# Kernel optimization log

Hardware: AMD Instinct MI355X
Metric: run time of the kernel (lower is better)

## Reference

```python
import jax, jax.numpy as jnp
import numpy as np
from jax import lax

DN = ('NHWC', 'HWIO', 'NHWC')


def conv_same(x, w):
    return lax.conv_general_dilated(x, w, window_strides=(1, 1), padding='SAME',
                                    dimension_numbers=DN)


def dwconv(x, w):
    # w: (kh, kw, F, 1) TF depthwise layout -> HWIO (kh, kw, 1, F), groups=F
    F = w.shape[2]
    return lax.conv_general_dilated(x, jnp.transpose(w, (0, 1, 3, 2)),
                                    window_strides=(1, 1), padding='SAME',
                                    dimension_numbers=DN, feature_group_count=F)


def hard_sigmoid(x):
    return jnp.clip(0.2 * x + 0.5, 0.0, 1.0)


def setup_inputs() -> dict:
    key = jax.random.key(0)
    ks = jax.random.split(key, 10)
    B, H, W, Cin, F = 16, 128, 128, 64, 64
    s = 0.05
    return {
        'inputs': jax.random.normal(ks[0], (B, H, W, Cin), jnp.float32),
        'h0': jax.random.normal(ks[1], (B, H, W, F), jnp.float32),
        'c0': jax.random.normal(ks[2], (B, H, W, F), jnp.float32),
        'm0': jax.random.normal(ks[3], (B, H, W, F), jnp.float32),
        'kernel': jax.random.normal(ks[4], (3, 3, Cin, 4 * F), jnp.float32) * s,
        'recurrent_kernel': jax.random.normal(ks[5], (3, 3, F, 4 * F), jnp.float32) * s,
        'bias': jnp.concatenate([jnp.zeros((F,), jnp.float32),
                                 jnp.ones((F,), jnp.float32),
                                 jnp.zeros((2 * F,), jnp.float32)]),
        'sa_kernel': jax.random.normal(ks[6], (1, 1, F, 5), jnp.float32) * s,
        'kernel_z': jax.random.normal(ks[7], (3, 3, 2, F), jnp.float32) * s,
        'depth_wise_kernel': jax.random.normal(ks[8], (3, 3, F, 6), jnp.float32) * s,
        'sa_bias': jnp.zeros((3 * F,), jnp.float32),
    }


def reference(inputs, h0, c0, m0, kernel, recurrent_kernel, bias, sa_kernel,
              kernel_z, depth_wise_kernel, sa_bias):
    F = h0.shape[-1]
    # --- ConvLSTM gates (no dropout: all four gates share the same input, so
    # a single fused conv over the 4F-channel kernel is the same math) ---
    xz = conv_same(inputs, kernel) + bias  # [B,H,W,4F]
    hz = conv_same(h0, recurrent_kernel)   # [B,H,W,4F]
    z = xz + hz
    zi_, zf_, zc_, zo_ = jnp.split(z, 4, axis=-1)
    i = hard_sigmoid(zi_)
    f = hard_sigmoid(zf_)
    c = f * c0 + i * jnp.tanh(zc_)
    o = hard_sigmoid(zo_)
    h = o * jnp.tanh(c)  # [B,H,W,F]

    # --- Self-attention memory (SAM) module; 1x1 convs -> channel contractions ---
    w = sa_kernel[0, 0]  # [F,5]
    v_h = jnp.einsum('bhwc,c->bhw', h, w[:, 0])
    k_h = jnp.einsum('bhwc,c->bhw', h, w[:, 1])
    q_h = jnp.einsum('bhwc,c->bhw', h, w[:, 2])
    k_m = jnp.einsum('bhwc,c->bhw', m0, w[:, 3])
    v_m = jnp.einsum('bhwc,c->bhw', m0, w[:, 4])

    alpha_m = jax.nn.softmax(jnp.matmul(q_h, k_m), axis=-1)  # [B,H,H] (H==W)
    alpha_h = jax.nn.softmax(jnp.matmul(q_h, k_h), axis=-1)
    z_m = jnp.matmul(alpha_m, v_m)  # [B,H,W]
    z_h = jnp.matmul(alpha_h, v_h)

    zi = conv_same(jnp.stack([z_h, z_m], axis=-1), kernel_z)  # [B,H,W,F]

    dw = depth_wise_kernel  # [3,3,F,6]
    b_i, b_g, b_o = jnp.split(sa_bias, 3)
    i2 = jax.nn.sigmoid(dwconv(zi, dw[..., 0:1]) + dwconv(h, dw[..., 1:2]) + b_i)
    g = jnp.tanh(dwconv(zi, dw[..., 2:3]) + dwconv(h, dw[..., 3:4]) + b_g)
    o2 = jax.nn.sigmoid(dwconv(zi, dw[..., 4:5]) + dwconv(h, dw[..., 5:6]) + b_o)

    m_t = (1.0 - i2) * m0 + i2 * g
    h_hat = m_t * o2
    return h_hat, c, m_t
```

## Files before the change

### kernel.cpp

```cpp
#include <hip/hip_runtime.h>

#define BB 16
#define HH 128
#define WW 128
#define FF 64
#define NPIX (BB*HH*WW)

typedef short bf16x8 __attribute__((ext_vector_type(8)));
typedef float f32x4 __attribute__((ext_vector_type(4)));

__device__ __forceinline__ float bf2f(unsigned int u){ return __uint_as_float(u<<16); }
__device__ __forceinline__ unsigned short f2bf(float f){
  unsigned u = __float_as_uint(f);
  u += 0x7fffu + ((u>>16)&1u);
  return (unsigned short)(u>>16);
}
__device__ __forceinline__ float hsig(float x){ return fminf(fmaxf(fmaf(0.2f,x,0.5f),0.f),1.f); }
__device__ __forceinline__ float tanh_fast(float x){
  float e = __expf(2.f*x);
  return 1.f - 2.f/(e + 1.f);
}
__device__ __forceinline__ void gload_lds16(const void* g, void* l){
  __builtin_amdgcn_global_load_lds(
      (const __attribute__((address_space(1))) unsigned int*)g,
      (__attribute__((address_space(3))) unsigned int*)l, 16, 0, 0);
}

__global__ __launch_bounds__(256) void zero_pads(unsigned short* __restrict__ Xp){
  int i = blockIdx.x*256 + threadIdx.x;
  if (i >= 16*516) return;
  int b = i / 516, r = i % 516;
  int y, x;
  if (r < 130){ y = 0; x = r; }
  else if (r < 260){ y = 129; x = r-130; }
  else if (r < 388){ y = r-260+1; x = 0; }
  else { y = r-388+1; x = 129; }
  unsigned short* p = Xp + (((size_t)(b*130 + y)*130) + x)*128;
  uint4 z = {0u,0u,0u,0u};
  #pragma unroll
  for (int c=0;c<16;++c) ((uint4*)p)[c] = z;
}

__global__ __launch_bounds__(256) void prep_x(const float* __restrict__ in,
                                              const float* __restrict__ h0,
                                              unsigned short* __restrict__ Xp){
  int gi = blockIdx.x*256 + threadIdx.x;
  int pix = gi >> 4;
  int ch8 = (gi & 15) * 8;
  const float* src = (ch8 < 64) ? (in + (size_t)pix*64 + ch8)
                                : (h0 + (size_t)pix*64 + (ch8-64));
  float4 v0 = *(const float4*)src;
  float4 v1 = *(const float4*)(src+4);
  uint4 o;
  o.x = (unsigned)f2bf(v0.x) | ((unsigned)f2bf(v0.y)<<16);
  o.y = (unsigned)f2bf(v0.z) | ((unsigned)f2bf(v0.w)<<16);
  o.z = (unsigned)f2bf(v1.x) | ((unsigned)f2bf(v1.y)<<16);
  o.w = (unsigned)f2bf(v1.z) | ((unsigned)f2bf(v1.w)<<16);
  int b = pix >> 14, y = (pix >> 7) & 127, x = pix & 127;
  *(uint4*)(Xp + (((size_t)(b*130 + y+1)*130) + (x+1))*128 + ch8) = o;
}

__global__ __launch_bounds__(256) void prep_w(const float* __restrict__ kern,
                                              const float* __restrict__ rkern,
                                              unsigned short* __restrict__ Wg){
  int k = blockIdx.x;
  int n = threadIdx.x;
  int tap = k >> 7, c = k & 127;
  float v = (c < 64) ? kern[((size_t)(tap*64 + c))*256 + n]
                     : rkern[((size_t)(tap*64 + (c-64)))*256 + n];
  Wg[(size_t)n*1152 + k] = f2bf(v);
}

__global__ __launch_bounds__(256, 2) void gates_kernel(
    const unsigned short* __restrict__ Xp,
    const unsigned short* __restrict__ Wg,
    const float* __restrict__ bias,
    const float* __restrict__ c0,
    float* __restrict__ c_out,
    unsigned short* __restrict__ h_bf){
  __shared__ unsigned short As[2][130*128];
  const int gid = blockIdx.x;
  const int swz = (gid & 7)*256 + (gid >> 3);
  const int b  = swz >> 7;
  const int y  = swz & 127;
  const int tid = threadIdx.x;
  const int l = tid & 63;
  const int wid = tid >> 6;
  const int l15 = l & 15, l4 = l >> 4;
  const int n0 = wid*16 + l15;

  const unsigned short* brow[4];
  #pragma unroll
  for (int g=0; g<4; ++g) brow[g] = Wg + (size_t)(g*64 + n0)*1152 + l4*8;

  f32x4 acc[8][4];
  #pragma unroll
  for (int mf=0;mf<8;++mf)
    #pragma unroll
    for (int g=0;g<4;++g) acc[mf][g] = (f32x4){0.f,0.f,0.f,0.f};

  auto stage = [&](int buf, int dyi){
    const unsigned short* gbase = Xp + ((size_t)((b*130 + y + dyi)*130))*128;
    unsigned short* lbase = &As[buf][0];
    #pragma unroll
    for (int it=0; it<8; ++it){
      int q = it*256 + tid;
      int px = q >> 4, c = q & 15;
      int cs = c ^ (px & 7);
      gload_lds16(gbase + (size_t)px*128 + cs*8, lbase + (size_t)q*8);
    }
    if (l < 8){
      int q = 2048 + wid*8 + l;
      int px = q >> 4, c = q & 15;
      int cs = c ^ (px & 7);
      gload_lds16(gbase + (size_t)px*128 + cs*8, lbase + (size_t)q*8);
    }
  };

  stage(0, 0);
  for (int dyi = 0; dyi < 3; ++dyi){
    if (dyi < 2){
      stage((dyi+1)&1, dyi+1);
      asm volatile("s_waitcnt vmcnt(9)" ::: "memory");
    } else {
      asm volatile("s_waitcnt vmcnt(0)" ::: "memory");
    }
    __builtin_amdgcn_sched_barrier(0);
    __builtin_amdgcn_s_barrier();
    __builtin_amdgcn_sched_barrier(0);
    const unsigned short* asb = &As[dyi&1][0];
    #pragma unroll
    for (int dxi = 0; dxi < 3; ++dxi){
      const int tap = dyi*3 + dxi;
      #pragma unroll
      for (int ksc = 0; ksc < 2; ++ksc){
        bf16x8 bfr[4][2];
        #pragma unroll
        for (int g=0; g<4; ++g)
          #pragma unroll
          for (int k2=0; k2<2; ++k2)
            bfr[g][k2] = *(const bf16x8*)(brow[g] + tap*128 + (ksc*2+k2)*32);
        #pragma unroll
        for (int k2=0; k2<2; ++k2){
          const int cd = (ksc*2+k2)*4 + l4;
          #pragma unroll
          for (int mf=0; mf<8; ++mf){
            const int px = mf*16 + l15 + dxi;
            bf16x8 a = *(const bf16x8*)(asb + (size_t)px*128 + ((cd ^ (px & 7))*8));
            #pragma unroll
            for (int g=0;g<4;++g)
              acc[mf][g] = __builtin_amdgcn_mfma_f32_16x16x32_bf16(a, bfr[g][k2], acc[mf][g], 0,0,0);
          }
        }
      }
    }
    __builtin_amdgcn_sched_barrier(0);
    __builtin_amdgcn_s_barrier();
    __builtin_amdgcn_sched_barrier(0);
  }
  const float b0 = bias[n0], b1 = bias[64+n0], b2 = bias[128+n0], b3 = bias[192+n0];
  const size_t prow = (size_t)(b*128 + y)*128;
  #pragma unroll
  for (int mf=0;mf<8;++mf){
    #pragma unroll
    for (int r=0;r<4;++r){
      const int x = mf*16 + l4*4 + r;
      const size_t p = prow + x;
      const float zi_ = acc[mf][0][r] + b0;
      const float zf_ = acc[mf][1][r] + b1;
      const float zc_ = acc[mf][2][r] + b2;
      const float zo_ = acc[mf][3][r] + b3;
      const float iv = hsig(zi_), fv = hsig(zf_), ov = hsig(zo_);
      const float cv = fv*c0[p*64 + n0] + iv*tanh_fast(zc_);
      const float hv = ov*tanh_fast(cv);
      c_out[p*64 + n0] = cv;
      h_bf[p*64 + n0] = f2bf(hv);
    }
  }
}

__global__ __launch_bounds__(256) void qkv_kernel(
    const unsigned short* __restrict__ h_bf, const float* __restrict__ m0,
    const float* __restrict__ sak,
    float* __restrict__ q_h, float* __restrict__ k_h, float* __restrict__ v_h,
    float* __restrict__ k_m, float* __restrict__ v_m){
  __shared__ float wS[320];
  for (int i = threadIdx.x; i < 320; i += 256) wS[i] = sak[i];
  __syncthreads();
  const int p = blockIdx.x*256 + threadIdx.x;
  const unsigned short* hp = h_bf + (size_t)p*64;
  const float* mp = m0 + (size_t)p*64;
  float a0=0,a1=0,a2=0,a3=0,a4=0;
  #pragma unroll
  for (int ch = 0; ch < 64; ch += 8){
    uint4 hu = *(const uint4*)(hp + ch);
    float4 ma = *(const float4*)(mp + ch);
    float4 mb = *(const float4*)(mp + ch + 4);
    float hv[8] = { bf2f(hu.x&0xffffu), bf2f(hu.x>>16), bf2f(hu.y&0xffffu), bf2f(hu.y>>16),
                    bf2f(hu.z&0xffffu), bf2f(hu.z>>16), bf2f(hu.w&0xffffu), bf2f(hu.w>>16) };
    float mv[8] = { ma.x,ma.y,ma.z,ma.w, mb.x,mb.y,mb.z,mb.w };
    #pragma unroll
    for (int jj=0;jj<8;++jj){
      const float* w = &wS[(ch+jj)*5];
      a0 = fmaf(hv[jj], w[0], a0);
      a1 = fmaf(hv[jj], w[1], a1);
      a2 = fmaf(hv[jj], w[2], a2);
      a3 = fmaf(mv[jj], w[3], a3);
      a4 = fmaf(mv[jj], w[4], a4);
    }
  }
  v_h[p]=a0; k_h[p]=a1; q_h[p]=a2; k_m[p]=a3; v_m[p]=a4;
}

__global__ __launch_bounds__(256) void attn_kernel(
    const float* __restrict__ q_h, const float* __restrict__ k_h, const float* __restrict__ v_h,
    const float* __restrict__ k_m, const float* __restrict__ v_m,
    float* __restrict__ z_h, float* __restrict__ z_m){
  __shared__ float Kl[128][132];
  __shared__ float Vl[128][132];
  __shared__ float q2[8][132];
  __shared__ float al[8][132];
  const int bid = blockIdx.x;
  const int b = bid >> 4;
  const int type = (bid >> 3) & 1;
  const int rb = bid & 7;
  const float* K = (type ? k_m : k_h) + (size_t)b*16384;
  const float* V = (type ? v_m : v_h) + (size_t)b*16384;
  const float* Q = q_h + (size_t)b*16384;
  float* Z = (type ? z_m : z_h) + (size_t)b*16384;
  const int t = threadIdx.x;
  const int jq = t & 31;
  const int r8 = t >> 5;

  for (int base = 0; base < 16384; base += 1024){
    const int idx = base + t*4;
    const int w = idx >> 7, j = idx & 127;
    const float4 kv = *(const float4*)(K + idx);
    const float4 vv = *(const float4*)(V + idx);
    *(float4*)&Kl[w][j] = kv;
    *(float4*)&Vl[w][j] = vv;
  }

  for (int p = 0; p < 2; ++p){
    __syncthreads();
    for (int idx = t; idx < 1024; idx += 256)
      q2[idx>>7][idx&127] = Q[(rb*16 + p*8 + (idx>>7))*128 + (idx&127)];
    __syncthreads();
    const int i = rb*16 + p*8 + r8;
    float s0=0.f,s1=0.f,s2=0.f,s3=0.f;
    #pragma unroll 8
    for (int w=0; w<128; ++w){
      const float qv = q2[r8][w];
      const float4 kv = *(const float4*)&Kl[w][jq*4];
      s0 = fmaf(qv, kv.x, s0); s1 = fmaf(qv, kv.y, s1);
      s2 = fmaf(qv, kv.z, s2); s3 = fmaf(qv, kv.w, s3);
    }
    float mx = fmaxf(fmaxf(s0,s1), fmaxf(s2,s3));
    #pragma unroll
    for (int o=1;o<32;o<<=1) mx = fmaxf(mx, __shfl_xor(mx, o));
    const float p0 = __expf(s0-mx), p1 = __expf(s1-mx);
    const float p2 = __expf(s2-mx), p3 = __expf(s3-mx);
    float sm = (p0+p1)+(p2+p3);
    #pragma unroll
    for (int o=1;o<32;o<<=1) sm += __shfl_xor(sm, o);
    const float inv = 1.f/sm;
    *(float4*)&al[r8][jq*4] = make_float4(p0*inv, p1*inv, p2*inv, p3*inv);
    __syncthreads();
    float z0=0.f,z1=0.f,z2=0.f,z3=0.f;
    #pragma unroll 8
    for (int w=0; w<128; ++w){
      const float av = al[r8][w];
      const float4 vv = *(const float4*)&Vl[w][jq*4];
      z0 = fmaf(av, vv.x, z0); z1 = fmaf(av, vv.y, z1);
      z2 = fmaf(av, vv.z, z2); z3 = fmaf(av, vv.w, z3);
    }
    *(float4*)(Z + (size_t)i*128 + jq*4) = make_float4(z0,z1,z2,z3);
  }
}

__global__ __launch_bounds__(512) void final_fused(
    const float* __restrict__ z_h, const float* __restrict__ z_m,
    const float* __restrict__ kz,
    const unsigned short* __restrict__ h_bf,
    const float* __restrict__ m0, const float* __restrict__ dwk,
    const float* __restrict__ sab,
    float* __restrict__ hhat, float* __restrict__ m_t){
  __shared__ unsigned short zi[4][128][64];
  const int f = threadIdx.x & 63;
  const int g = threadIdx.x >> 6;
  const int blk = blockIdx.x;
  const int b = blk >> 6;
  const int y0 = (blk & 63) * 2;

  {
    const int ry = g >> 1;
    const int xh = g & 1;
    const int yy = y0 - 1 + ry;
    const int x0 = xh * 64;
    if ((unsigned)yy >= 128u){
      for (int i=0;i<64;++i) zi[ry][x0+i][f] = 0;
    } else {
      float w0[9], w1[9];
      #pragma unroll
      for (int tap=0; tap<9; ++tap){
        w0[tap] = kz[tap*128 + f];
        w1[tap] = kz[tap*128 + 64 + f];
      }
      const float* zhr = z_h + (size_t)(b*128 + yy)*128;
      const float* zmr = z_m + (size_t)(b*128 + yy)*128;
      const bool ym = (yy > 0), yp = (yy < 127);
      float az[3][3], am[3][3];
      auto ldc = [&](int x, float (&Z)[3], float (&M)[3]){
        if ((unsigned)x < 128u){
          Z[0] = ym ? zhr[x-128] : 0.f;  M[0] = ym ? zmr[x-128] : 0.f;
          Z[1] = zhr[x];                 M[1] = zmr[x];
          Z[2] = yp ? zhr[x+128] : 0.f;  M[2] = yp ? zmr[x+128] : 0.f;
        } else { Z[0]=Z[1]=Z[2]=0.f; M[0]=M[1]=M[2]=0.f; }
      };
      ldc(x0-1, az[0], am[0]);
      ldc(x0,   az[1], am[1]);
      for (int i=0; i<64; ++i){
        const int x = x0 + i;
        ldc(x+1, az[2], am[2]);
        float acc = 0.f;
        #pragma unroll
        for (int tap=0; tap<9; ++tap){
          const int dy = tap/3, dx = tap%3;
          acc = fmaf(az[dx][dy], w0[tap], acc);
          acc = fmaf(am[dx][dy], w1[tap], acc);
        }
        zi[ry][x][f] = f2bf(acc);
        #pragma unroll
        for (int k=0;k<3;++k){
          az[0][k]=az[1][k]; az[1][k]=az[2][k];
          am[0][k]=am[1][k]; am[1][k]=am[2][k];
        }
      }
    }
  }
  __syncthreads();

  const int r2 = g >> 2;
  const int xq = g & 3;
  const int y = y0 + r2;
  const size_t rb = (size_t)(b*128 + y)*128;
  float wv[9][6];
  #pragma unroll
  for (int tap=0;tap<9;++tap)
    #pragma unroll
    for (int jj=0;jj<6;++jj) wv[tap][jj] = dwk[(tap*64 + f)*6 + jj];
  const float bi = sab[f], bg = sab[64+f], bo = sab[128+f];
  const bool ym = (y > 0), yp = (y < 127);
  float vz[3][3], vh[3][3];
  auto ldc2 = [&](int x, float (&Z)[3], float (&H)[3]){
    if ((unsigned)x < 128u){
      const size_t base = (rb + x)*64 + f;
      H[0] = ym ? bf2f(h_bf[base - 8192]) : 0.f;
      H[1] = bf2f(h_bf[base]);
      H[2] = yp ? bf2f(h_bf[base + 8192]) : 0.f;
      Z[0] = bf2f(zi[r2  ][x][f]);
      Z[1] = bf2f(zi[r2+1][x][f]);
      Z[2] = bf2f(zi[r2+2][x][f]);
    } else { Z[0]=Z[1]=Z[2]=0.f; H[0]=H[1]=H[2]=0.f; }
  };
  const int x0 = xq*32;
  ldc2(x0-1, vz[0], vh[0]);
  ldc2(x0,   vz[1], vh[1]);
  for (int i=0; i<32; ++i){
    const int x = x0 + i;
    ldc2(x+1, vz[2], vh[2]);
    float si=0.f, sg=0.f, so=0.f;
    #pragma unroll
    for (int tap=0;tap<9;++tap){
      const int dy = tap/3, dx = tap%3;
      const float zv = vz[dx][dy], hv = vh[dx][dy];
      si = fmaf(zv, wv[tap][0], si); si = fmaf(hv, wv[tap][1], si);
      sg = fmaf(zv, wv[tap][2], sg); sg = fmaf(hv, wv[tap][3], sg);
      so = fmaf(zv, wv[tap][4], so); so = fmaf(hv, wv[tap][5], so);
    }
    const size_t p = rb + x;
    const float i2 = 1.f/(1.f+__expf(-(si+bi)));
    const float gg = tanh_fast(sg+bg);
    const float o2 = 1.f/(1.f+__expf(-(so+bo)));
    const float mv = m0[p*64+f];
    const float mt = (1.f-i2)*mv + i2*gg;
    hhat[p*64+f] = mt*o2;
    m_t[p*64+f]  = mt;
    #pragma unroll
    for (int k=0;k<3;++k){
      vz[0][k]=vz[1][k]; vz[1][k]=vz[2][k];
      vh[0][k]=vh[1][k]; vh[1][k]=vh[2][k];
    }
  }
}

extern "C" void kernel_launch(void* const* d_in, const int* in_sizes, int n_in,
                              void* d_out, int out_size, void* d_ws, size_t ws_size,
                              hipStream_t stream){
  const float* inputs = (const float*)d_in[0];
  const float* h0p    = (const float*)d_in[1];
  const float* c0p    = (const float*)d_in[2];
  const float* m0p    = (const float*)d_in[3];
  const float* kern   = (const float*)d_in[4];
  const float* rkern  = (const float*)d_in[5];
  const float* biasp  = (const float*)d_in[6];
  const float* sakp   = (const float*)d_in[7];
  const float* kzp    = (const float*)d_in[8];
  const float* dwkp   = (const float*)d_in[9];
  const float* sabp   = (const float*)d_in[10];
  float* out = (float*)d_out;
  char* ws = (char*)d_ws;

  constexpr size_t SZ_XP  = (size_t)16*130*130*128*2;
  constexpr size_t SZ_WG  = (size_t)256*1152*2;
  constexpr size_t SZ_HBF = (size_t)NPIX*64*2;
  constexpr size_t SZA    = (size_t)NPIX*4;
  constexpr size_t OFF_XP  = 0;
  constexpr size_t OFF_WG  = OFF_XP + SZ_XP;
  constexpr size_t OFF_HBF = OFF_WG + SZ_WG;
  constexpr size_t OFF_Q   = OFF_HBF + SZ_HBF;
  constexpr size_t OFF_KH  = OFF_Q  + SZA;
  constexpr size_t OFF_VH  = OFF_KH + SZA;
  constexpr size_t OFF_KM  = OFF_VH + SZA;
  constexpr size_t OFF_VM  = OFF_KM + SZA;
  constexpr size_t OFF_ZH  = OFF_VM + SZA;
  constexpr size_t OFF_ZM  = OFF_ZH + SZA;

  unsigned short* Xp  = (unsigned short*)(ws + OFF_XP);
  unsigned short* Wg  = (unsigned short*)(ws + OFF_WG);
  unsigned short* Hbf = (unsigned short*)(ws + OFF_HBF);
  float* Qh = (float*)(ws + OFF_Q);
  float* Kh = (float*)(ws + OFF_KH);
  float* Vh = (float*)(ws + OFF_VH);
  float* Km = (float*)(ws + OFF_KM);
  float* Vm = (float*)(ws + OFF_VM);
  float* Zh = (float*)(ws + OFF_ZH);
  float* Zm = (float*)(ws + OFF_ZM);

  zero_pads<<<33, 256, 0, stream>>>(Xp);
  prep_x<<<NPIX*16/256, 256, 0, stream>>>(inputs, h0p, Xp);
  prep_w<<<1152, 256, 0, stream>>>(kern, rkern, Wg);
  gates_kernel<<<2048, 256, 0, stream>>>(Xp, Wg, biasp, c0p,
                                         out + (size_t)NPIX*64, Hbf);
  qkv_kernel<<<NPIX/256, 256, 0, stream>>>(Hbf, m0p, sakp, Qh, Kh, Vh, Km, Vm);
  attn_kernel<<<256, 256, 0, stream>>>(Qh, Kh, Vh, Km, Vm, Zh, Zm);
  final_fused<<<1024, 512, 0, stream>>>(Zh, Zm, kzp, Hbf, m0p, dwkp, sabp,
                                        out, out + 2*(size_t)NPIX*64);
}
```

Measured before the change: 409.4 us.

## Fuse QKV projection into attention kernel and merge prep kernels

Merges the three preprocessing kernels (pad zeroing, input conversion to bf16, weight transpose) into a single launch that dispatches by block index. Removes the separate qkv projection kernel: the attention kernel now computes the K/V projections for a whole image directly into shared memory and computes Q rows on the fly. This drops the intermediate Q/K/V global buffers and two launches. In exchange, the attention grid shrinks from 256 to 64 blocks, and each block rereads a full image of h or m0 with per-thread strided loads. That risks low GPU occupancy and poorly coalesced memory traffic.

Measured after the change: 590.8 us. 44.3% more time.

```diff
diff --git a/kernel.cpp b/kernel.cpp
--- a/kernel.cpp
+++ b/kernel.cpp
@@ -26,49 +26,48 @@
       (__attribute__((address_space(3))) unsigned int*)l, 16, 0, 0);
 }
 
-__global__ __launch_bounds__(256) void zero_pads(unsigned short* __restrict__ Xp){
-  int i = blockIdx.x*256 + threadIdx.x;
-  if (i >= 16*516) return;
-  int b = i / 516, r = i % 516;
-  int y, x;
-  if (r < 130){ y = 0; x = r; }
-  else if (r < 260){ y = 129; x = r-130; }
-  else if (r < 388){ y = r-260+1; x = 0; }
-  else { y = r-388+1; x = 129; }
-  unsigned short* p = Xp + (((size_t)(b*130 + y)*130) + x)*128;
-  uint4 z = {0u,0u,0u,0u};
-  #pragma unroll
-  for (int c=0;c<16;++c) ((uint4*)p)[c] = z;
-}
-
-__global__ __launch_bounds__(256) void prep_x(const float* __restrict__ in,
-                                              const float* __restrict__ h0,
-                                              unsigned short* __restrict__ Xp){
-  int gi = blockIdx.x*256 + threadIdx.x;
-  int pix = gi >> 4;
-  int ch8 = (gi & 15) * 8;
-  const float* src = (ch8 < 64) ? (in + (size_t)pix*64 + ch8)
-                                : (h0 + (size_t)pix*64 + (ch8-64));
-  float4 v0 = *(const float4*)src;
-  float4 v1 = *(const float4*)(src+4);
-  uint4 o;
-  o.x = (unsigned)f2bf(v0.x) | ((unsigned)f2bf(v0.y)<<16);
-  o.y = (unsigned)f2bf(v0.z) | ((unsigned)f2bf(v0.w)<<16);
-  o.z = (unsigned)f2bf(v1.x) | ((unsigned)f2bf(v1.y)<<16);
-  o.w = (unsigned)f2bf(v1.z) | ((unsigned)f2bf(v1.w)<<16);
-  int b = pix >> 14, y = (pix >> 7) & 127, x = pix & 127;
-  *(uint4*)(Xp + (((size_t)(b*130 + y+1)*130) + (x+1))*128 + ch8) = o;
-}
-
-__global__ __launch_bounds__(256) void prep_w(const float* __restrict__ kern,
-                                              const float* __restrict__ rkern,
-                                              unsigned short* __restrict__ Wg){
-  int k = blockIdx.x;
-  int n = threadIdx.x;
-  int tap = k >> 7, c = k & 127;
-  float v = (c < 64) ? kern[((size_t)(tap*64 + c))*256 + n]
-                     : rkern[((size_t)(tap*64 + (c-64)))*256 + n];
-  Wg[(size_t)n*1152 + k] = f2bf(v);
+__global__ __launch_bounds__(256) void prep_all(
+    const float* __restrict__ in, const float* __restrict__ h0,
+    const float* __restrict__ kern, const float* __restrict__ rkern,
+    unsigned short* __restrict__ Xp, unsigned short* __restrict__ Wg){
+  const int blk = blockIdx.x;
+  const int t = threadIdx.x;
+  if (blk < 33){
+    int i = blk*256 + t;
+    if (i >= 16*516) return;
+    int b = i / 516, r = i % 516;
+    int y, x;
+    if (r < 130){ y = 0; x = r; }
+    else if (r < 260){ y = 129; x = r-130; }
+    else if (r < 388){ y = r-260+1; x = 0; }
+    else { y = r-388+1; x = 129; }
+    unsigned short* p = Xp + (((size_t)(b*130 + y)*130) + x)*128;
+    uint4 z = {0u,0u,0u,0u};
+    #pragma unroll
+    for (int c=0;c<16;++c) ((uint4*)p)[c] = z;
+  } else if (blk < 33 + 16384){
+    int gi = (blk-33)*256 + t;
+    int pix = gi >> 4;
+    int ch8 = (gi & 15) * 8;
+    const float* src = (ch8 < 64) ? (in + (size_t)pix*64 + ch8)
+                                  : (h0 + (size_t)pix*64 + (ch8-64));
+    float4 v0 = *(const float4*)src;
+    float4 v1 = *(const float4*)(src+4);
+    uint4 o;
+    o.x = (unsigned)f2bf(v0.x) | ((unsigned)f2bf(v0.y)<<16);
+    o.y = (unsigned)f2bf(v0.z) | ((unsigned)f2bf(v0.w)<<16);
+    o.z = (unsigned)f2bf(v1.x) | ((unsigned)f2bf(v1.y)<<16);
+    o.w = (unsigned)f2bf(v1.z) | ((unsigned)f2bf(v1.w)<<16);
+    int b = pix >> 14, y = (pix >> 7) & 127, x = pix & 127;
+    *(uint4*)(Xp + (((size_t)(b*130 + y+1)*130) + (x+1))*128 + ch8) = o;
+  } else {
+    int k = blk - (33 + 16384);
+    int n = t;
+    int tap = k >> 7, c = k & 127;
+    float v = (c < 64) ? kern[((size_t)(tap*64 + c))*256 + n]
+                       : rkern[((size_t)(tap*64 + (c-64)))*256 + n];
+    Wg[(size_t)n*1152 + k] = f2bf(v);
+  }
 }
 
 __global__ __launch_bounds__(256, 2) void gates_kernel(
@@ -179,74 +178,82 @@
   }
 }
 
-__global__ __launch_bounds__(256) void qkv_kernel(
+__global__ __launch_bounds__(256) void attn_kernel(
     const unsigned short* __restrict__ h_bf, const float* __restrict__ m0,
     const float* __restrict__ sak,
-    float* __restrict__ q_h, float* __restrict__ k_h, float* __restrict__ v_h,
-    float* __restrict__ k_m, float* __restrict__ v_m){
-  __shared__ float wS[320];
-  for (int i = threadIdx.x; i < 320; i += 256) wS[i] = sak[i];
-  __syncthreads();
-  const int p = blockIdx.x*256 + threadIdx.x;
-  const unsigned short* hp = h_bf + (size_t)p*64;
-  const float* mp = m0 + (size_t)p*64;
-  float a0=0,a1=0,a2=0,a3=0,a4=0;
-  #pragma unroll
-  for (int ch = 0; ch < 64; ch += 8){
-    uint4 hu = *(const uint4*)(hp + ch);
-    float4 ma = *(const float4*)(mp + ch);
-    float4 mb = *(const float4*)(mp + ch + 4);
-    float hv[8] = { bf2f(hu.x&0xffffu), bf2f(hu.x>>16), bf2f(hu.y&0xffffu), bf2f(hu.y>>16),
-                    bf2f(hu.z&0xffffu), bf2f(hu.z>>16), bf2f(hu.w&0xffffu), bf2f(hu.w>>16) };
-    float mv[8] = { ma.x,ma.y,ma.z,ma.w, mb.x,mb.y,mb.z,mb.w };
-    #pragma unroll
-    for (int jj=0;jj<8;++jj){
-      const float* w = &wS[(ch+jj)*5];
-      a0 = fmaf(hv[jj], w[0], a0);
-      a1 = fmaf(hv[jj], w[1], a1);
-      a2 = fmaf(hv[jj], w[2], a2);
-      a3 = fmaf(mv[jj], w[3], a3);
-      a4 = fmaf(mv[jj], w[4], a4);
-    }
-  }
-  v_h[p]=a0; k_h[p]=a1; q_h[p]=a2; k_m[p]=a3; v_m[p]=a4;
-}
-
-__global__ __launch_bounds__(256) void attn_kernel(
-    const float* __restrict__ q_h, const float* __restrict__ k_h, const float* __restrict__ v_h,
-    const float* __restrict__ k_m, const float* __restrict__ v_m,
     float* __restrict__ z_h, float* __restrict__ z_m){
   __shared__ float Kl[128][132];
   __shared__ float Vl[128][132];
   __shared__ float q2[8][132];
   __shared__ float al[8][132];
+  __shared__ float wS[320];
   const int bid = blockIdx.x;
-  const int b = bid >> 4;
-  const int type = (bid >> 3) & 1;
-  const int rb = bid & 7;
-  const float* K = (type ? k_m : k_h) + (size_t)b*16384;
-  const float* V = (type ? v_m : v_h) + (size_t)b*16384;
-  const float* Q = q_h + (size_t)b*16384;
-  float* Z = (type ? z_m : z_h) + (size_t)b*16384;
+  const int b = bid >> 2;
+  const int type = (bid >> 1) & 1;
+  const int rh = bid & 1;
   const int t = threadIdx.x;
   const int jq = t & 31;
   const int r8 = t >> 5;
-
-  for (int base = 0; base < 16384; base += 1024){
-    const int idx = base + t*4;
-    const int w = idx >> 7, j = idx & 127;
-    const float4 kv = *(const float4*)(K + idx);
-    const float4 vv = *(const float4*)(V + idx);
-    *(float4*)&Kl[w][j] = kv;
-    *(float4*)&Vl[w][j] = vv;
-  }
-
-  for (int p = 0; p < 2; ++p){
+  for (int i = t; i < 320; i += 256) wS[i] = sak[i];
+  __syncthreads();
+  const unsigned short* hB = h_bf + (size_t)b*16384*64;
+  const float* mB = m0 + (size_t)b*16384*64;
+  float* Z = (type ? z_m : z_h) + (size_t)b*16384;
+
+  for (int base = 0; base < 16384; base += 256){
+    const int p = base + t;
+    float kv = 0.f, vv = 0.f;
+    if (type == 0){
+      const unsigned short* hp = hB + (size_t)p*64;
+      #pragma unroll
+      for (int ch = 0; ch < 64; ch += 8){
+        uint4 hu = *(const uint4*)(hp + ch);
+        float hv[8] = { bf2f(hu.x&0xffffu), bf2f(hu.x>>16), bf2f(hu.y&0xffffu), bf2f(hu.y>>16),
+                        bf2f(hu.z&0xffffu), bf2f(hu.z>>16), bf2f(hu.w&0xffffu), bf2f(hu.w>>16) };
+        #pragma unroll
+        for (int jj=0;jj<8;++jj){
+          kv = fmaf(hv[jj], wS[(ch+jj)*5 + 1], kv);
+          vv = fmaf(hv[jj], wS[(ch+jj)*5 + 0], vv);
+        }
+      }
+    } else {
+      const float* mp = mB + (size_t)p*64;
+      #pragma unroll
+      for (int ch = 0; ch < 64; ch += 8){
+        float4 ma = *(const float4*)(mp + ch);
+        float4 mb2 = *(const float4*)(mp + ch + 4);
+        float mv[8] = { ma.x,ma.y,ma.z,ma.w, mb2.x,mb2.y,mb2.z,mb2.w };
+        #pragma unroll
+        for (int jj=0;jj<8;++jj){
+          kv = fmaf(mv[jj], wS[(ch+jj)*5 + 3], kv);
+          vv = fmaf(mv[jj], wS[(ch+jj)*5 + 4], vv);
+        }
+      }
+    }
+    Kl[p>>7][p&127] = kv;
+    Vl[p>>7][p&127] = vv;
+  }
+
+  for (int pass = 0; pass < 8; ++pass){
     __syncthreads();
-    for (int idx = t; idx < 1024; idx += 256)
-      q2[idx>>7][idx&127] = Q[(rb*16 + p*8 + (idx>>7))*128 + (idx&127)];
+    for (int idx = t; idx < 1024; idx += 256){
+      const int rr = idx >> 7, j = idx & 127;
+      const int p = (rh*64 + pass*8 + rr)*128 + j;
+      const unsigned short* hp = hB + (size_t)p*64;
+      float qv = 0.f;
+      #pragma unroll
+      for (int ch = 0; ch < 64; ch += 8){
+        uint4 hu = *(const uint4*)(hp + ch);
+        float hv[8] = { bf2f(hu.x&0xffffu), bf2f(hu.x>>16), bf2f(hu.y&0xffffu), bf2f(hu.y>>16),
+                        bf2f(hu.z&0xffffu), bf2f(hu.z>>16), bf2f(hu.w&0xffffu), bf2f(hu.w>>16) };
+        #pragma unroll
+        for (int jj=0;jj<8;++jj)
+          qv = fmaf(hv[jj], wS[(ch+jj)*5 + 2], qv);
+      }
+      q2[rr][j] = qv;
+    }
     __syncthreads();
-    const int i = rb*16 + p*8 + r8;
+    const int i = rh*64 + pass*8 + r8;
     float s0=0.f,s1=0.f,s2=0.f,s3=0.f;
     #pragma unroll 8
     for (int w=0; w<128; ++w){
@@ -418,32 +425,19 @@
   constexpr size_t OFF_XP  = 0;
   constexpr size_t OFF_WG  = OFF_XP + SZ_XP;
   constexpr size_t OFF_HBF = OFF_WG + SZ_WG;
-  constexpr size_t OFF_Q   = OFF_HBF + SZ_HBF;
-  constexpr size_t OFF_KH  = OFF_Q  + SZA;
-  constexpr size_t OFF_VH  = OFF_KH + SZA;
-  constexpr size_t OFF_KM  = OFF_VH + SZA;
-  constexpr size_t OFF_VM  = OFF_KM + SZA;
-  constexpr size_t OFF_ZH  = OFF_VM + SZA;
+  constexpr size_t OFF_ZH  = OFF_HBF + SZ_HBF;
   constexpr size_t OFF_ZM  = OFF_ZH + SZA;
 
   unsigned short* Xp  = (unsigned short*)(ws + OFF_XP);
   unsigned short* Wg  = (unsigned short*)(ws + OFF_WG);
   unsigned short* Hbf = (unsigned short*)(ws + OFF_HBF);
-  float* Qh = (float*)(ws + OFF_Q);
-  float* Kh = (float*)(ws + OFF_KH);
-  float* Vh = (float*)(ws + OFF_VH);
-  float* Km = (float*)(ws + OFF_KM);
-  float* Vm = (float*)(ws + OFF_VM);
   float* Zh = (float*)(ws + OFF_ZH);
   float* Zm = (float*)(ws + OFF_ZM);
 
-  zero_pads<<<33, 256, 0, stream>>>(Xp);
-  prep_x<<<NPIX*16/256, 256, 0, stream>>>(inputs, h0p, Xp);
-  prep_w<<<1152, 256, 0, stream>>>(kern, rkern, Wg);
+  prep_all<<<33 + 16384 + 1152, 256, 0, stream>>>(inputs, h0p, kern, rkern, Xp, Wg);
   gates_kernel<<<2048, 256, 0, stream>>>(Xp, Wg, biasp, c0p,
                                          out + (size_t)NPIX*64, Hbf);
-  qkv_kernel<<<NPIX/256, 256, 0, stream>>>(Hbf, m0p, sakp, Qh, Kh, Vh, Km, Vm);
-  attn_kernel<<<256, 256, 0, stream>>>(Qh, Kh, Vh, Km, Vm, Zh, Zm);
+  attn_kernel<<<64, 256, 0, stream>>>(Hbf, m0p, sakp, Zh, Zm);
   final_fused<<<1024, 512, 0, stream>>>(Zh, Zm, kzp, Hbf, m0p, dwkp, sabp,
                                         out, out + 2*(size_t)NPIX*64);
 }
```
